# Performance work log

Hardware: AMD Instinct MI355X
Metric: run time of the kernel (lower is better)

Reference implementation:

```python
import jax, jax.numpy as jnp
import numpy as np

B, N, S = 8, 8192, 2048
IN, SKIP, OUT, EXP = 256, 128, 256, 4
GROUPS = 8


def conv1d(x, w, b):
    # 1x1 conv: x [B,C,N], w [O,C], b [O]
    return jnp.einsum('bcn,oc->bon', x, w) + b[None, :, None]


def group_norm(x, w, b, groups=GROUPS, eps=1e-5):
    Bb, C, Nn = x.shape
    xg = x.reshape(Bb, groups, C // groups, Nn)
    m = xg.mean(axis=(2, 3), keepdims=True)
    v = xg.var(axis=(2, 3), keepdims=True)
    xn = ((xg - m) * jax.lax.rsqrt(v + eps)).reshape(Bb, C, Nn)
    return xn * w[None, :, None] + b[None, :, None]


def _forward(xyz1, points1, xyz2, points2, t_emb, c_emb,
             mlp_w, mlp_b, mlp_gw, mlp_gb,
             c1w, c1b, g1w, g1b, c2w, c2b, g2w, g2b,
             tw, tb, cw, cb):
    # pairwise squared distances [B,N,S]
    dists = (-2.0 * jnp.einsum('bcn,bcm->bnm', xyz1, xyz2)
             + jnp.sum(xyz1 ** 2, axis=1)[:, :, None]
             + jnp.sum(xyz2 ** 2, axis=1)[:, None, :])
    neg_d3, idx = jax.lax.top_k(-dists, 3)          # 3 smallest distances
    d3 = -neg_d3                                     # [B,N,3]
    recip = 1.0 / (d3 + 1e-8)
    weight = recip / jnp.sum(recip, axis=2, keepdims=True)
    # gather neighbor features: points2 [B,C,S], idx [B,N,3] -> [B,C,N,3]
    gathered = jax.vmap(lambda p, i: p[:, i])(points2, idx)
    interp = jnp.sum(gathered * weight[:, None, :, :], axis=3)  # [B,IN,N]

    new_points = jnp.concatenate([points1, interp], axis=1)     # [B,IN+SKIP,N]
    x = jax.nn.silu(group_norm(conv1d(new_points, mlp_w, mlp_b), mlp_gw, mlp_gb))

    identity = x
    h = jax.nn.silu(group_norm(conv1d(x, c1w, c1b), g1w, g1b))
    h = group_norm(conv1d(h, c2w, c2b), g2w, g2b)
    st = t_emb @ tw.T + tb
    sc = c_emb @ cw.T + cb
    scale_t, shift_t = jnp.split(st, 2, axis=1)
    scale_c, shift_c = jnp.split(sc, 2, axis=1)
    scale = (scale_t + scale_c)[:, :, None]
    shift = (shift_t + shift_c)[:, :, None]
    h = h * (1.0 + scale) + shift
    return h + identity


def setup_inputs() -> dict:
    key = jax.random.key(0)
    ks = jax.random.split(key, 12)
    def rn(k, shape, s=1.0):
        return jax.random.normal(k, shape, dtype=jnp.float32) * s
    E = OUT * EXP
    return dict(
        xyz1=rn(ks[0], (B, 3, N)),
        points1=rn(ks[1], (B, SKIP, N)),
        xyz2=rn(ks[2], (B, 3, S)),
        points2=rn(ks[3], (B, IN, S)),
        t_emb=rn(ks[4], (B, OUT)),
        c_emb=rn(ks[5], (B, OUT)),
        mlp_w=rn(ks[6], (OUT, IN + SKIP), 0.02), mlp_b=jnp.zeros((OUT,), jnp.float32),
        mlp_gw=jnp.ones((OUT,), jnp.float32), mlp_gb=jnp.zeros((OUT,), jnp.float32),
        c1w=rn(ks[7], (E, OUT), 0.02), c1b=jnp.zeros((E,), jnp.float32),
        g1w=jnp.ones((E,), jnp.float32), g1b=jnp.zeros((E,), jnp.float32),
        c2w=rn(ks[8], (OUT, E), 0.02), c2b=jnp.zeros((OUT,), jnp.float32),
        g2w=jnp.ones((OUT,), jnp.float32), g2b=jnp.zeros((OUT,), jnp.float32),
        tw=rn(ks[9], (2 * OUT, OUT), 0.02), tb=jnp.zeros((2 * OUT,), jnp.float32),
        cw=rn(ks[10], (2 * OUT, OUT), 0.02), cb=jnp.zeros((2 * OUT,), jnp.float32),
    )


def reference(xyz1, points1, xyz2, points2, t_emb, c_emb,
              mlp_w, mlp_b, mlp_gw, mlp_gb,
              c1w, c1b, g1w, g1b, c2w, c2b, g2w, g2b,
              tw, tb, cw, cb):
    return _forward(xyz1, points1, xyz2, points2, t_emb, c_emb,
                    mlp_w, mlp_b, mlp_gw, mlp_gb,
                    c1w, c1b, g1w, g1b, c2w, c2b, g2w, g2b,
                    tw, tb, cw, cb)
```

## Files before the change

### kernel.cpp

```cpp
#include <hip/hip_runtime.h>
#include <hip/hip_bf16.h>

typedef unsigned short u16;
typedef __attribute__((ext_vector_type(4))) float f32x4;
typedef __attribute__((ext_vector_type(8))) short bf16x8;

typedef const __attribute__((address_space(1))) void GV;
typedef __attribute__((address_space(3))) void LV;
#define GLOAD16(g, l) __builtin_amdgcn_global_load_lds((GV*)(g), (LV*)(l), 16, 0, 0)

__device__ __forceinline__ float b2f(u16 u) {
    union { float f; unsigned int i; } v; v.i = ((unsigned int)u) << 16; return v.f;
}
__device__ __forceinline__ u16 f2b(float f) {
    union { float f; unsigned int i; } v; v.f = f;
    unsigned int x = v.i;
    return (u16)((x + 0x7fffu + ((x >> 16) & 1u)) >> 16);
}
__device__ __forceinline__ unsigned int cvt_pk_bf16(float lo, float hi) {
    unsigned int d;
    asm("v_cvt_pk_bf16_f32 %0, %1, %2" : "=v"(d) : "v"(lo), "v"(hi));
    return d;
}

__global__ void knn_part_kernel(const float* __restrict__ xyz1, const float* __restrict__ xyz2,
                                float2* __restrict__ cand) {
    __shared__ float4 spt[256];
    int b = blockIdx.z, ck = blockIdx.y, tid = threadIdx.x;
    const float* p2 = xyz2 + (size_t)b * 3 * 2048;
    int s0 = ck << 8;
    {
        int s = s0 + tid;
        float x = p2[s], y = p2[2048 + s], z = p2[4096 + s];
        spt[tid] = make_float4(x, y, z, (x * x + y * y) + z * z);
    }
    __syncthreads();
    int n = blockIdx.x * 256 + tid;
    const float* p1 = xyz1 + (size_t)b * 3 * 8192;
    float qx = p1[n], qy = p1[8192 + n], qz = p1[16384 + n];
    float qn = (qx * qx + qy * qy) + qz * qz;
    float d0 = 3.4e38f, d1 = 3.4e38f, d2 = 3.4e38f;
    int i0 = 0, i1 = 0, i2 = 0;
#pragma unroll 4
    for (int s = 0; s < 256; ++s) {
        float4 p = spt[s];
        float dot = (qx * p.x + qy * p.y) + qz * p.z;
        float d = (-2.f * dot + qn) + p.w;
        if (d < d2) {
            int gi = s0 + s;
            if (d < d1) {
                if (d < d0) { d2 = d1; i2 = i1; d1 = d0; i1 = i0; d0 = d; i0 = gi; }
                else        { d2 = d1; i2 = i1; d1 = d;  i1 = gi; }
            } else          { d2 = d;  i2 = gi; }
        }
    }
    float2* c = cand + (((size_t)b * 8192 + n) * 8 + ck) * 3;
    c[0] = make_float2(d0, __int_as_float(i0));
    c[1] = make_float2(d1, __int_as_float(i1));
    c[2] = make_float2(d2, __int_as_float(i2));
}

__global__ void knn_merge_kernel(const float2* __restrict__ cand,
                                 int* __restrict__ idx_out, float* __restrict__ w_out) {
    int t = blockIdx.x * 256 + threadIdx.x;
    const float2* c = cand + (size_t)t * 24;
    float d0 = 3.4e38f, d1 = 3.4e38f, d2 = 3.4e38f;
    int i0 = 0, i1 = 0, i2 = 0;
#pragma unroll
    for (int k = 0; k < 24; ++k) {
        float2 p = c[k];
        float d = p.x;
        if (d < d2) {
            int gi = __float_as_int(p.y);
            if (d < d1) {
                if (d < d0) { d2 = d1; i2 = i1; d1 = d0; i1 = i0; d0 = d; i0 = gi; }
                else        { d2 = d1; i2 = i1; d1 = d;  i1 = gi; }
            } else          { d2 = d;  i2 = gi; }
        }
    }
    float r0 = 1.f / (d0 + 1e-8f), r1 = 1.f / (d1 + 1e-8f), r2 = 1.f / (d2 + 1e-8f);
    float inv = 1.f / (r0 + r1 + r2);
    size_t base = (size_t)t * 3;
    idx_out[base] = i0; idx_out[base + 1] = i1; idx_out[base + 2] = i2;
    w_out[base] = r0 * inv; w_out[base + 1] = r1 * inv; w_out[base + 2] = r2 * inv;
}

__global__ void tr_kernel(const float* __restrict__ src, u16* __restrict__ dst, int C, int S) {
    __shared__ u16 tile[64][70];
    int b = blockIdx.z;
    int s0 = blockIdx.x * 64, c0 = blockIdx.y * 64;
    int tid = threadIdx.x, lane = tid & 63, wv = tid >> 6;
    const float* sp = src + ((size_t)b * C + c0) * S + s0;
    for (int c = wv; c < 64; c += 4)
        tile[lane][c] = f2b(sp[(size_t)c * S + lane]);
    __syncthreads();
    u16* dp = dst + ((size_t)b * S + s0) * C + c0;
    int s = tid >> 5, cp = tid & 31;
#pragma unroll
    for (int k = 0; k < 8; ++k) {
        int r = s + k * 8;
        unsigned int v = *(const unsigned int*)&tile[r][cp * 2];
        *(unsigned int*)&dp[(size_t)r * C + cp * 2] = v;
    }
}

__global__ void build_x0_kernel(const u16* __restrict__ p1t, const u16* __restrict__ p2t,
                                const int* __restrict__ idx, const float* __restrict__ wgt,
                                u16* __restrict__ x0t) {
    int b = blockIdx.y;
    int n = blockIdx.x * 64 + (threadIdx.x >> 2);
    int q = threadIdx.x & 3;
    size_t ib = ((size_t)b * 8192 + n) * 3;
    int j0 = idx[ib], j1 = idx[ib + 1], j2 = idx[ib + 2];
    float w0 = wgt[ib], w1 = wgt[ib + 1], w2 = wgt[ib + 2];
    const u16* pr = p1t + ((size_t)b * 8192 + n) * 128;
    const u16* r0 = p2t + ((size_t)b * 2048 + j0) * 256;
    const u16* r1 = p2t + ((size_t)b * 2048 + j1) * 256;
    const u16* r2 = p2t + ((size_t)b * 2048 + j2) * 256;
    u16* out = x0t + ((size_t)b * 8192 + n) * 384;
#pragma unroll
    for (int i = 0; i < 4; ++i) {
        int ch = (i * 4 + q) * 8;
        *(uint4*)&out[ch] = *(const uint4*)&pr[ch];
    }
#pragma unroll
    for (int i = 0; i < 8; ++i) {
        int c = (i * 4 + q) * 8;
        bf16x8 a0 = *(const bf16x8*)&r0[c];
        bf16x8 a1 = *(const bf16x8*)&r1[c];
        bf16x8 a2 = *(const bf16x8*)&r2[c];
        u16 ovu[8] __attribute__((aligned(16)));
#pragma unroll
        for (int j = 0; j < 8; ++j) {
            float v = w0 * b2f((u16)a0[j]) + w1 * b2f((u16)a1[j]) + w2 * b2f((u16)a2[j]);
            ovu[j] = f2b(v);
        }
        *(uint4*)&out[128 + c] = *(const uint4*)ovu;
    }
}

__global__ void cvt_kernel(const float* __restrict__ src, u16* __restrict__ dst, int n) {
    int i = blockIdx.x * 256 + threadIdx.x;
    if (i < n) dst[i] = f2b(src[i]);
}

__global__ void film_kernel(const float* __restrict__ t_emb, const float* __restrict__ c_emb,
                            const float* __restrict__ tw, const float* __restrict__ tb,
                            const float* __restrict__ cw, const float* __restrict__ cb,
                            float* __restrict__ film) {
    __shared__ float te[256], ce[256];
    int b = blockIdx.x, tid = threadIdx.x;
    te[tid] = t_emb[b * 256 + tid];
    ce[tid] = c_emb[b * 256 + tid];
    __syncthreads();
    int j = tid + blockIdx.y * 256;
    const float* twr = tw + (size_t)j * 256;
    const float* cwr = cw + (size_t)j * 256;
    float s = 0.f;
    for (int k = 0; k < 256; ++k) s += te[k] * twr[k] + ce[k] * cwr[k];
    s += tb[j] + cb[j];
    film[b * 512 + j] = s;
}

__global__ __launch_bounds__(256) void gemm_kernel(
        const u16* __restrict__ At, const u16* __restrict__ W, const float* __restrict__ bias,
        u16* __restrict__ Out, float* __restrict__ part,
        int K, int M, int gshift) {
    __shared__ u16 lA[128 * 64];
    __shared__ u16 lB[128 * 64];
    __shared__ float bpart[4][2];
    int b = blockIdx.z;
    int n0 = blockIdx.x * 128, o0 = blockIdx.y * 128;
    int tid = threadIdx.x, lane = tid & 63, wv = tid >> 6;
    int wn = wv & 1, wo = wv >> 1;
    if (tid < 8) ((float*)bpart)[tid] = 0.f;
    f32x4 acc[4][4];
#pragma unroll
    for (int i = 0; i < 4; i++)
#pragma unroll
        for (int j = 0; j < 4; j++) acc[i][j] = (f32x4){0.f, 0.f, 0.f, 0.f};

    int rl = lane >> 3;
    int csw = ((lane & 7) ^ rl) * 8;
    const u16* aP[4];
    const u16* bP[4];
#pragma unroll
    for (int p4 = 0; p4 < 4; p4++) {
        int p = wv * 4 + p4;
        aP[p4] = At + ((size_t)b * 8192 + n0 + p * 8 + rl) * K + csw;
        bP[p4] = W + ((size_t)(o0 + p * 8 + rl)) * K + csw;
    }
    int nK = K >> 6;
    for (int kt = 0; kt < nK; ++kt) {
#pragma unroll
        for (int p4 = 0; p4 < 4; p4++) {
            int p = wv * 4 + p4;
            GLOAD16(aP[p4], &lA[p * 512]);
            GLOAD16(bP[p4], &lB[p * 512]);
            aP[p4] += 64; bP[p4] += 64;
        }
        __syncthreads();
#pragma unroll
        for (int kk = 0; kk < 2; kk++) {
            bf16x8 af[4], bfr[4];
#pragma unroll
            for (int mf = 0; mf < 4; mf++) {
                int R = wn * 64 + mf * 16 + (lane & 15);
                af[mf] = *(const bf16x8*)&lA[R * 64 + ((kk * 4 + (lane >> 4)) ^ (R & 7)) * 8];
            }
#pragma unroll
            for (int nf = 0; nf < 4; nf++) {
                int R = wo * 64 + nf * 16 + (lane & 15);
                bfr[nf] = *(const bf16x8*)&lB[R * 64 + ((kk * 4 + (lane >> 4)) ^ (R & 7)) * 8];
            }
#pragma unroll
            for (int mf = 0; mf < 4; mf++)
#pragma unroll
                for (int nf = 0; nf < 4; nf++)
                    acc[mf][nf] = __builtin_amdgcn_mfma_f32_16x16x32_bf16(bfr[nf], af[mf], acc[mf][nf], 0, 0, 0);
        }
        __syncthreads();
    }
    int oq = (lane >> 4) * 4;
    float4 bs[4];
    float s1[4] = {0.f, 0.f, 0.f, 0.f}, s2[4] = {0.f, 0.f, 0.f, 0.f};
#pragma unroll
    for (int nf = 0; nf < 4; nf++) bs[nf] = *(const float4*)&bias[o0 + wo * 64 + nf * 16 + oq];
#pragma unroll
    for (int mf = 0; mf < 4; mf++) {
        int n = n0 + wn * 64 + mf * 16 + (lane & 15);
        u16* rowp = Out + ((size_t)b * 8192 + n) * M + o0 + wo * 64 + oq;
#pragma unroll
        for (int nf = 0; nf < 4; nf++) {
            float v0 = acc[mf][nf][0] + bs[nf].x;
            float v1 = acc[mf][nf][1] + bs[nf].y;
            float v2 = acc[mf][nf][2] + bs[nf].z;
            float v3 = acc[mf][nf][3] + bs[nf].w;
            s1[nf] += (v0 + v1) + (v2 + v3);
            s2[nf] += (v0 * v0 + v1 * v1) + (v2 * v2 + v3 * v3);
            uint2 pk;
            pk.x = cvt_pk_bf16(v0, v1);
            pk.y = cvt_pk_bf16(v2, v3);
            *(uint2*)&rowp[nf * 16] = pk;
        }
    }
#pragma unroll
    for (int nf = 0; nf < 4; nf++) {
        float a = s1[nf], c = s2[nf];
#pragma unroll
        for (int off = 32; off > 0; off >>= 1) {
            a += __shfl_xor(a, off, 64);
            c += __shfl_xor(c, off, 64);
        }
        if (lane == 0) {
            int gl = (wo * 64 + nf * 16) >> gshift;
            atomicAdd(&bpart[gl][0], a);
            atomicAdd(&bpart[gl][1], c);
        }
    }
    __syncthreads();
    int nlg = 128 >> gshift;
    if (tid < 2 * nlg) {
        int gl = tid >> 1, s = tid & 1;
        int g = (o0 >> gshift) + gl;
        part[(((size_t)b * 8 + g) * 2 + s) * 64 + blockIdx.x] = bpart[gl][s];
    }
}

__global__ void gn_reduce_kernel(const float* __restrict__ part, float* __restrict__ stats) {
    int t = threadIdx.x;
    const float4* p = (const float4*)(part + (size_t)t * 64);
    float s = 0.f;
#pragma unroll
    for (int i = 0; i < 16; i++) { float4 v = p[i]; s += (v.x + v.y) + (v.z + v.w); }
    stats[t] = s;
}

__global__ void gn_act2_kernel(u16* __restrict__ Y, const float* __restrict__ gw,
                               const float* __restrict__ gb, const float* __restrict__ stats,
                               int c8bits, int gshift, float invCnt) {
    int t = blockIdx.x * 256 + threadIdx.x;
    int C8m = (1 << c8bits) - 1;
    int c8 = t & C8m;
    int c0 = c8 << 3;
    int g = c0 >> gshift;
    int row0 = t >> c8bits;
    int rowstep = (gridDim.x * 256) >> c8bits;
    float4 w0 = *(const float4*)(gw + c0), w1 = *(const float4*)(gw + c0 + 4);
    float4 b0 = *(const float4*)(gb + c0), b1 = *(const float4*)(gb + c0 + 4);
    float wv[8] = {w0.x, w0.y, w0.z, w0.w, w1.x, w1.y, w1.z, w1.w};
    float bv[8] = {b0.x, b0.y, b0.z, b0.w, b1.x, b1.y, b1.z, b1.w};
    float A[8], Bc[8];
    int bprev = -1;
    for (int row = row0; row < 65536; row += rowstep) {
        int b = row >> 13;
        if (b != bprev) {
            bprev = b;
            float sum = stats[(b * 8 + g) * 2], ssq = stats[(b * 8 + g) * 2 + 1];
            float m = sum * invCnt;
            float rstd = rsqrtf(fmaxf(ssq * invCnt - m * m, 0.f) + 1e-5f);
#pragma unroll
            for (int j = 0; j < 8; j++) { A[j] = rstd * wv[j]; Bc[j] = bv[j] - m * rstd * wv[j]; }
        }
        u16* p = Y + (((size_t)row << c8bits) << 3) + c0;
        uint4 v4 = *(const uint4*)p;
        u16* vu = (u16*)&v4;
#pragma unroll
        for (int j = 0; j < 8; j++) {
            float v = b2f(vu[j]) * A[j] + Bc[j];
            v = v * __builtin_amdgcn_rcpf(1.f + __expf(-v));
            vu[j] = f2b(v);
        }
        *(uint4*)p = v4;
    }
}

__global__ void final_kernel(const u16* __restrict__ Y2, const u16* __restrict__ X,
                             const float* __restrict__ g2w, const float* __restrict__ g2b,
                             const float* __restrict__ stats, const float* __restrict__ film,
                             float* __restrict__ out) {
    __shared__ float tile[64][257];
    int b = blockIdx.y, n0 = blockIdx.x * 64, tid = threadIdx.x;
    const float invCnt = 1.f / (32.f * 8192.f);
    int c8 = tid & 31, c0 = c8 << 3, g = c8 >> 2;
    float sum = stats[(b * 8 + g) * 2], ssq = stats[(b * 8 + g) * 2 + 1];
    float m = sum * invCnt, rstd = rsqrtf(fmaxf(ssq * invCnt - m * m, 0.f) + 1e-5f);
    float4 w0 = *(const float4*)(g2w + c0), w1 = *(const float4*)(g2w + c0 + 4);
    float4 q0 = *(const float4*)(g2b + c0), q1 = *(const float4*)(g2b + c0 + 4);
    float4 f0 = *(const float4*)(film + b * 512 + c0), f1 = *(const float4*)(film + b * 512 + c0 + 4);
    float4 h0 = *(const float4*)(film + b * 512 + 256 + c0), h1 = *(const float4*)(film + b * 512 + 256 + c0 + 4);
    float wv[8] = {w0.x, w0.y, w0.z, w0.w, w1.x, w1.y, w1.z, w1.w};
    float qv[8] = {q0.x, q0.y, q0.z, q0.w, q1.x, q1.y, q1.z, q1.w};
    float fs[8] = {f0.x, f0.y, f0.z, f0.w, f1.x, f1.y, f1.z, f1.w};
    float fh[8] = {h0.x, h0.y, h0.z, h0.w, h1.x, h1.y, h1.z, h1.w};
    float A[8], Bc[8];
#pragma unroll
    for (int j = 0; j < 8; j++) {
        float sc = 1.f + fs[j];
        A[j] = rstd * wv[j] * sc;
        Bc[j] = (qv[j] - m * rstd * wv[j]) * sc + fh[j];
    }
    int nrb = tid >> 5;
#pragma unroll
    for (int k = 0; k < 8; k++) {
        int nr = nrb + k * 8;
        size_t base = ((size_t)b * 8192 + n0 + nr) * 256 + c0;
        uint4 yv = *(const uint4*)(Y2 + base);
        uint4 xv = *(const uint4*)(X + base);
        const u16* yy = (const u16*)&yv;
        const u16* xx = (const u16*)&xv;
#pragma unroll
        for (int j = 0; j < 8; j++)
            tile[nr][c0 + j] = b2f(yy[j]) * A[j] + Bc[j] + b2f(xx[j]);
    }
    __syncthreads();
    for (int q = tid; q < 256 * 16; q += 256) {
        int c = q >> 4, n4 = q & 15;
        float4 o;
        o.x = tile[n4 * 4 + 0][c];
        o.y = tile[n4 * 4 + 1][c];
        o.z = tile[n4 * 4 + 2][c];
        o.w = tile[n4 * 4 + 3][c];
        *(float4*)&out[((size_t)b * 256 + c) * 8192 + n0 + n4 * 4] = o;
    }
}

extern "C" void kernel_launch(void* const* d_in, const int* in_sizes, int n_in,
                              void* d_out, int out_size, void* d_ws, size_t ws_size,
                              hipStream_t stream) {
    const float* xyz1    = (const float*)d_in[0];
    const float* points1 = (const float*)d_in[1];
    const float* xyz2    = (const float*)d_in[2];
    const float* points2 = (const float*)d_in[3];
    const float* t_emb   = (const float*)d_in[4];
    const float* c_emb   = (const float*)d_in[5];
    const float* mlp_w   = (const float*)d_in[6];
    const float* mlp_b   = (const float*)d_in[7];
    const float* mlp_gw  = (const float*)d_in[8];
    const float* mlp_gb  = (const float*)d_in[9];
    const float* c1w     = (const float*)d_in[10];
    const float* c1b     = (const float*)d_in[11];
    const float* g1w     = (const float*)d_in[12];
    const float* g1b     = (const float*)d_in[13];
    const float* c2w     = (const float*)d_in[14];
    const float* c2b     = (const float*)d_in[15];
    const float* g2w     = (const float*)d_in[16];
    const float* g2b     = (const float*)d_in[17];
    const float* tw      = (const float*)d_in[18];
    const float* tb      = (const float*)d_in[19];
    const float* cw      = (const float*)d_in[20];
    const float* cb      = (const float*)d_in[21];

    char* ws = (char*)d_ws;
    int*   idx    = (int*)ws;
    float* wgt    = (float*)(ws + 786432);
    float* stats0 = (float*)(ws + 1572864);
    float* stats1 = (float*)(ws + 1573376);
    float* stats2 = (float*)(ws + 1573888);
    float* film   = (float*)(ws + 1574400);
    float* part0  = (float*)(ws + 1590784);
    float* part1  = (float*)(ws + 1623552);
    float* part2  = (float*)(ws + 1656320);
    u16* wb_mlp   = (u16*)(ws + 1689088);
    u16* wb_c1    = (u16*)(ws + 1885696);
    u16* wb_c2    = (u16*)(ws + 2409984);
    u16* X0t = (u16*)(ws + 4194304);
    u16* Y1t = (u16*)(ws + 54525952);
    u16* H1t = (u16*)(ws + 88080384);
    u16* Y2t = X0t;
    float2* cand = (float2*)X0t;
    u16* p1t = H1t;
    u16* p2t = H1t + 8388608ull;
    float* out = (float*)d_out;

    cvt_kernel<<<384, 256, 0, stream>>>(mlp_w, wb_mlp, 98304);
    cvt_kernel<<<1024, 256, 0, stream>>>(c1w, wb_c1, 262144);
    cvt_kernel<<<1024, 256, 0, stream>>>(c2w, wb_c2, 262144);
    knn_part_kernel<<<dim3(32, 8, 8), 256, 0, stream>>>(xyz1, xyz2, cand);
    knn_merge_kernel<<<256, 256, 0, stream>>>(cand, idx, wgt);
    tr_kernel<<<dim3(128, 2, 8), 256, 0, stream>>>(points1, p1t, 128, 8192);
    tr_kernel<<<dim3(32, 4, 8), 256, 0, stream>>>(points2, p2t, 256, 2048);
    build_x0_kernel<<<dim3(128, 8), 256, 0, stream>>>(p1t, p2t, idx, wgt, X0t);
    film_kernel<<<dim3(8, 2), 256, 0, stream>>>(t_emb, c_emb, tw, tb, cw, cb, film);
    gemm_kernel<<<dim3(64, 2, 8), 256, 0, stream>>>(X0t, wb_mlp, mlp_b, Y1t, part0, 384, 256, 5);
    gn_reduce_kernel<<<1, 128, 0, stream>>>(part0, stats0);
    gn_act2_kernel<<<512, 256, 0, stream>>>(Y1t, mlp_gw, mlp_gb, stats0, 5, 5, 1.f / (32.f * 8192.f));
    gemm_kernel<<<dim3(64, 8, 8), 256, 0, stream>>>(Y1t, wb_c1, c1b, H1t, part1, 256, 1024, 7);
    gn_reduce_kernel<<<1, 128, 0, stream>>>(part1, stats1);
    gn_act2_kernel<<<2048, 256, 0, stream>>>(H1t, g1w, g1b, stats1, 7, 7, 1.f / (128.f * 8192.f));
    gemm_kernel<<<dim3(64, 2, 8), 256, 0, stream>>>(H1t, wb_c2, c2b, Y2t, part2, 1024, 256, 5);
    gn_reduce_kernel<<<1, 128, 0, stream>>>(part2, stats2);
    final_kernel<<<dim3(128, 8), 256, 0, stream>>>(Y2t, Y1t, g2w, g2b, stats2, film, out);
}
```

Measured before the change: 395.3 us.

## Double-buffer LDS tiles in GEMM to overlap global loads with MFMA

Splits the shared A/B tiles into two buffers. The next K-tile is prefetched with global_load_lds while MFMAs run on the current one, and each iteration ends with a single barrier. This aims to hide global memory latency that was previously exposed before each compute step. The cost is doubled LDS use (64KB), which may lower occupancy. The manual waitcnt and barrier placement also needs to be right to avoid races.

```diff
diff --git a/kernel.cpp b/kernel.cpp
--- a/kernel.cpp
+++ b/kernel.cpp
@@ -166,8 +166,8 @@
         const u16* __restrict__ At, const u16* __restrict__ W, const float* __restrict__ bias,
         u16* __restrict__ Out, float* __restrict__ part,
         int K, int M, int gshift) {
-    __shared__ u16 lA[128 * 64];
-    __shared__ u16 lB[128 * 64];
+    __shared__ u16 lA[2][128 * 64];
+    __shared__ u16 lB[2][128 * 64];
     __shared__ float bpart[4][2];
     int b = blockIdx.z;
     int n0 = blockIdx.x * 128, o0 = blockIdx.y * 128;
@@ -191,27 +191,40 @@
         bP[p4] = W + ((size_t)(o0 + p * 8 + rl)) * K + csw;
     }
     int nK = K >> 6;
+#pragma unroll
+    for (int p4 = 0; p4 < 4; p4++) {
+        int p = wv * 4 + p4;
+        GLOAD16(aP[p4], &lA[0][p * 512]);
+        GLOAD16(bP[p4], &lB[0][p * 512]);
+        aP[p4] += 64; bP[p4] += 64;
+    }
+    asm volatile("s_waitcnt vmcnt(0) lgkmcnt(0)" ::: "memory");
+    __builtin_amdgcn_s_barrier();
+    int cur = 0;
     for (int kt = 0; kt < nK; ++kt) {
-#pragma unroll
-        for (int p4 = 0; p4 < 4; p4++) {
-            int p = wv * 4 + p4;
-            GLOAD16(aP[p4], &lA[p * 512]);
-            GLOAD16(bP[p4], &lB[p * 512]);
-            aP[p4] += 64; bP[p4] += 64;
-        }
-        __syncthreads();
+        if (kt + 1 < nK) {
+#pragma unroll
+            for (int p4 = 0; p4 < 4; p4++) {
+                int p = wv * 4 + p4;
+                GLOAD16(aP[p4], &lA[cur ^ 1][p * 512]);
+                GLOAD16(bP[p4], &lB[cur ^ 1][p * 512]);
+                aP[p4] += 64; bP[p4] += 64;
+            }
+        }
+        const u16* la = lA[cur];
+        const u16* lb = lB[cur];
 #pragma unroll
         for (int kk = 0; kk < 2; kk++) {
             bf16x8 af[4], bfr[4];
 #pragma unroll
             for (int mf = 0; mf < 4; mf++) {
                 int R = wn * 64 + mf * 16 + (lane & 15);
-                af[mf] = *(const bf16x8*)&lA[R * 64 + ((kk * 4 + (lane >> 4)) ^ (R & 7)) * 8];
+                af[mf] = *(const bf16x8*)&la[R * 64 + ((kk * 4 + (lane >> 4)) ^ (R & 7)) * 8];
             }
 #pragma unroll
             for (int nf = 0; nf < 4; nf++) {
                 int R = wo * 64 + nf * 16 + (lane & 15);
-                bfr[nf] = *(const bf16x8*)&lB[R * 64 + ((kk * 4 + (lane >> 4)) ^ (R & 7)) * 8];
+                bfr[nf] = *(const bf16x8*)&lb[R * 64 + ((kk * 4 + (lane >> 4)) ^ (R & 7)) * 8];
             }
 #pragma unroll
             for (int mf = 0; mf < 4; mf++)
@@ -219,7 +232,10 @@
                 for (int nf = 0; nf < 4; nf++)
                     acc[mf][nf] = __builtin_amdgcn_mfma_f32_16x16x32_bf16(bfr[nf], af[mf], acc[mf][nf], 0, 0, 0);
         }
-        __syncthreads();
+        if (kt + 1 < nK)
+            asm volatile("s_waitcnt vmcnt(0)" ::: "memory");
+        __builtin_amdgcn_s_barrier();
+        cur ^= 1;
     }
     int oq = (lane >> 4) * 4;
     float4 bs[4];
```

New measurement: 388.6 us. Within noise of the previous version (-1.7%).
